# Kernel optimization log

Hardware: AMD Instinct MI355X
Metric: run time of the kernel (lower is better)

The kernel has to match this reference:

```python
import jax, jax.numpy as jnp
import numpy as np

N = 20000       # nodes
E = 320000      # edges
D_IN = 128
H = 512
OUT = 7
EPS = 1e-5


def setup_inputs() -> dict:
    key = jax.random.key(0)
    ks = jax.random.split(key, 16)
    def lin(k, fan_in, fan_out):
        bound = 1.0 / np.sqrt(fan_in)
        kw, kb = jax.random.split(k)
        W = jax.random.uniform(kw, (fan_in, fan_out), jnp.float32, -bound, bound)
        b = jax.random.uniform(kb, (fan_out,), jnp.float32, -bound, bound)
        return W, b
    x = jax.random.normal(ks[0], (N, D_IN), jnp.float32)
    edge_index = jax.random.randint(ks[1], (2, E), 0, N, dtype=jnp.int64)
    W1, b1 = lin(ks[2], D_IN, H)
    W2, b2 = lin(ks[3], H, H)
    W3, b3 = lin(ks[4], H, H)
    W4, b4 = lin(ks[5], H, H)
    ln_gamma = jnp.ones((H,), jnp.float32)
    ln_beta = jnp.zeros((H,), jnp.float32)
    W_out, b_out = lin(ks[6], H, OUT)
    return {"x": x, "edge_index": edge_index,
            "W1": W1, "b1": b1, "W2": W2, "b2": b2,
            "W3": W3, "b3": b3, "W4": W4, "b4": b4,
            "ln_gamma": ln_gamma, "ln_beta": ln_beta,
            "W_out": W_out, "b_out": b_out}


def _gcn_layer(x, W, b, src, dst, dinv):
    # transform, then symmetric-normalized gather/scatter-add (PyG GCNConv)
    h = x @ W                                    # [N, H]
    norm = dinv[src] * dinv[dst]                 # [E+N]
    msg = h[src] * norm[:, None]                 # gather + scale
    agg = jax.ops.segment_sum(msg, dst, num_segments=N)
    return agg + b


def reference(x, edge_index, W1, b1, W2, b2, W3, b3, W4, b4,
              ln_gamma, ln_beta, W_out, b_out):
    loops = jnp.arange(N, dtype=edge_index.dtype)
    src = jnp.concatenate([edge_index[0], loops])  # A + I self loops
    dst = jnp.concatenate([edge_index[1], loops])
    deg = jax.ops.segment_sum(jnp.ones_like(src, dtype=x.dtype), dst,
                              num_segments=N)
    dinv = jnp.where(deg > 0, jax.lax.rsqrt(deg), 0.0)

    def ln(h):
        mu = h.mean(-1, keepdims=True)
        var = h.var(-1, keepdims=True)
        return (h - mu) * jax.lax.rsqrt(var + EPS) * ln_gamma + ln_beta

    for W, b in ((W1, b1), (W2, b2), (W3, b3), (W4, b4)):
        x = jax.nn.relu(ln(_gcn_layer(x, W, b, src, dst, dinv)))
    g = x.mean(axis=0)           # mean pool over nodes -> [H]
    # dropout is identity in eval mode
    return g @ W_out + b_out     # [OUT]
```

## Files before the change

### kernel.cpp

```cpp
#include <hip/hip_runtime.h>

#define HID 512
#define OUTD 7
#define EPSV 1e-5f
#define PB 256
#define PR 32

typedef __attribute__((ext_vector_type(8))) short bf16x8;
typedef __attribute__((ext_vector_type(4))) float f32x4;
typedef __attribute__((ext_vector_type(2))) float f32x2;
typedef unsigned short ushort_t;
typedef unsigned int uint_t;
typedef unsigned char uchar_t;

__device__ __forceinline__ ushort_t f2bf(float f) {
    uint_t u = __float_as_uint(f);
    u = (u + 0x7fffu + ((u >> 16) & 1u)) >> 16;
    return (ushort_t)u;
}
__device__ __forceinline__ float bflo(uint_t u) { return __uint_as_float(u << 16); }
__device__ __forceinline__ float bfhi(uint_t u) { return __uint_as_float(u & 0xffff0000u); }

__device__ __forceinline__ void dec4(uint_t v, float* f) {
    f32x2 p0 = __builtin_amdgcn_cvt_pk_f32_fp8(v, false);
    f32x2 p1 = __builtin_amdgcn_cvt_pk_f32_fp8(v, true);
    f[0] = p0.x; f[1] = p0.y; f[2] = p1.x; f[3] = p1.y;
}
__device__ __forceinline__ uint_t enc4(float a, float b, float c, float d) {
    uint_t r = __builtin_amdgcn_cvt_pk_fp8_f32(a, b, 0, false);
    r = __builtin_amdgcn_cvt_pk_fp8_f32(c, d, r, true);
    return r;
}

__device__ __forceinline__ void gload_lds16(const ushort_t* g, ushort_t* l) {
    __builtin_amdgcn_global_load_lds(
        (const __attribute__((address_space(1))) uint_t*)g,
        (__attribute__((address_space(3))) uint_t*)l, 16, 0, 0);
}
__device__ __forceinline__ void gload_lds16_u8(const uchar_t* g, uchar_t* l) {
    __builtin_amdgcn_global_load_lds(
        (const __attribute__((address_space(1))) uint_t*)g,
        (__attribute__((address_space(3))) uint_t*)l, 16, 0, 0);
}


__global__ void zero_deg(int* __restrict__ deg, int N) {
    int i = blockIdx.x * blockDim.x + threadIdx.x;
    if (i < N) deg[i] = 0;
}

__global__ void setup2(const int* __restrict__ dst, int* __restrict__ deg, int E,
                       const float* __restrict__ W0, const float* __restrict__ W1,
                       const float* __restrict__ W2, const float* __restrict__ W3,
                       ushort_t* __restrict__ T0, ushort_t* __restrict__ T1,
                       ushort_t* __restrict__ T2, ushort_t* __restrict__ T3) {
    int i = blockIdx.x * blockDim.x + threadIdx.x;
    if (i < E) { atomicAdd(&deg[dst[i]], 1); return; }
    i -= E;
    const int S0 = 128 * HID, S1 = HID * HID;
    if (i < S0) { int k = i / HID, n = i % HID; T0[(size_t)n * 128 + k] = f2bf(W0[i]); return; }
    i -= S0;
    if (i < S1) { int k = i / HID, n = i % HID; T1[(size_t)n * HID + k] = f2bf(W1[i]); return; }
    i -= S1;
    if (i < S1) { int k = i / HID, n = i % HID; T2[(size_t)n * HID + k] = f2bf(W2[i]); return; }
    i -= S1;
    if (i < S1) { int k = i / HID, n = i % HID; T3[(size_t)n * HID + k] = f2bf(W3[i]); }
}


__global__ void scan1(const int* __restrict__ deg, int* __restrict__ off,
                      int* __restrict__ partial, float* __restrict__ dinv, int N) {
    __shared__ int s[256];
    const int t = threadIdx.x;
    const int i = blockIdx.x * 256 + t;
    int d = (i < N) ? deg[i] : 0;
    if (i < N) dinv[i] = rsqrtf((float)(d + 1));
    s[t] = d;
    __syncthreads();
#pragma unroll
    for (int ofs = 1; ofs < 256; ofs <<= 1) {
        int v = (t >= ofs) ? s[t - ofs] : 0;
        __syncthreads();
        s[t] += v;
        __syncthreads();
    }
    if (i < N) off[i] = s[t] - d;
    if (t == 255) partial[blockIdx.x] = s[255];
}

__global__ void scan23(int* __restrict__ off, const int* __restrict__ partial,
                       int* __restrict__ cursor, int N, int E, int nb) {
    __shared__ int s[256];
    __shared__ int ex[256];
    const int t = threadIdx.x;
    int d = (t < nb) ? partial[t] : 0;
    s[t] = d;
    __syncthreads();
#pragma unroll
    for (int ofs = 1; ofs < 256; ofs <<= 1) {
        int v = (t >= ofs) ? s[t - ofs] : 0;
        __syncthreads();
        s[t] += v;
        __syncthreads();
    }
    ex[t] = s[t] - d;
    __syncthreads();
    int i = blockIdx.x * 256 + t;
    if (i < N) {
        int v = off[i] + ex[i >> 8];
        off[i] = v;
        cursor[i] = v;
    } else if (i == N) {
        off[N] = E;
    }
}


__global__ void fill_cvt(const int* __restrict__ src, const int* __restrict__ dst,
                         int* __restrict__ cursor, int* __restrict__ srcs, int E,
                         const float* __restrict__ x, const float* __restrict__ dinv,
                         ushort_t* __restrict__ xb, int pairs) {
    int i = blockIdx.x * blockDim.x + threadIdx.x;
    if (i < E) { int p = atomicAdd(&cursor[dst[i]], 1); srcs[p] = src[i]; return; }
    i -= E;
    if (i < pairs) {
        float dr = dinv[i >> 6];
        float a = x[2 * i] * dr, b = x[2 * i + 1] * dr;
        uint_t d = __builtin_amdgcn_cvt_pk_fp8_f32(a, b, 0, false);
        xb[i] = (ushort_t)(d & 0xffffu);
    }
}


__global__ __launch_bounds__(256) void csr_agg_512(
        const uchar_t* __restrict__ xs, const int* __restrict__ off,
        const int* __restrict__ srcs, const float* __restrict__ dinv,
        uchar_t* __restrict__ ax, int N) {
    int gtid = blockIdx.x * 256 + threadIdx.x;
    int r = gtid >> 6, lane = gtid & 63;
    if (r >= N) return;
    const int half = lane >> 5, l32 = lane & 31;
    const uint4* xb = (const uint4*)xs;
    float a[16];
    if (half == 0) {
        uint4 v = xb[(size_t)r * 32 + l32];
        dec4(v.x, a); dec4(v.y, a + 4); dec4(v.z, a + 8); dec4(v.w, a + 12);
    } else {
#pragma unroll
        for (int q = 0; q < 16; q++) a[q] = 0.f;
    }
    int e = off[r];
    const int e1 = off[r + 1];
    for (; e + 8 <= e1; e += 8) {
        int si[4]; uint4 vi[4];
#pragma unroll
        for (int j = 0; j < 4; j++) si[j] = srcs[e + 2 * j + half];
#pragma unroll
        for (int j = 0; j < 4; j++) vi[j] = xb[(size_t)si[j] * 32 + l32];
#pragma unroll
        for (int j = 0; j < 4; j++) {
            float f[16];
            dec4(vi[j].x, f); dec4(vi[j].y, f + 4); dec4(vi[j].z, f + 8); dec4(vi[j].w, f + 12);
#pragma unroll
            for (int q = 0; q < 16; q++) a[q] += f[q];
        }
    }
    for (; e < e1; e += 2) {
        int idx = e + half;
        bool valid = idx < e1;
        int s = srcs[valid ? idx : e];
        uint4 v = xb[(size_t)s * 32 + l32];
        if (!valid) { v.x = 0; v.y = 0; v.z = 0; v.w = 0; }
        float f[16];
        dec4(v.x, f); dec4(v.y, f + 4); dec4(v.z, f + 8); dec4(v.w, f + 12);
#pragma unroll
        for (int q = 0; q < 16; q++) a[q] += f[q];
    }
#pragma unroll
    for (int q = 0; q < 16; q++) a[q] += __shfl_xor(a[q], 32);
    if (half == 0) {
        float dr = dinv[r];
        uint4 o;
        o.x = enc4(a[0] * dr,  a[1] * dr,  a[2] * dr,  a[3] * dr);
        o.y = enc4(a[4] * dr,  a[5] * dr,  a[6] * dr,  a[7] * dr);
        o.z = enc4(a[8] * dr,  a[9] * dr,  a[10] * dr, a[11] * dr);
        o.w = enc4(a[12] * dr, a[13] * dr, a[14] * dr, a[15] * dr);
        ((uint4*)ax)[(size_t)r * 32 + l32] = o;
    }
}

__global__ __launch_bounds__(256) void csr_agg_128(
        const uchar_t* __restrict__ xs, const int* __restrict__ off,
        const int* __restrict__ srcs, const float* __restrict__ dinv,
        uchar_t* __restrict__ ax, int N) {
    int gtid = blockIdx.x * 256 + threadIdx.x;
    int r = gtid >> 6, lane = gtid & 63;
    if (r >= N) return;
    const int sub = lane >> 3, l8 = lane & 7;
    const uint4* xb = (const uint4*)xs;
    float a[16];
    if (sub == 0) {
        uint4 v = xb[(size_t)r * 8 + l8];
        dec4(v.x, a); dec4(v.y, a + 4); dec4(v.z, a + 8); dec4(v.w, a + 12);
    } else {
#pragma unroll
        for (int q = 0; q < 16; q++) a[q] = 0.f;
    }
    const int e1 = off[r + 1];
    for (int e = off[r]; e < e1; e += 8) {
        int idx = e + sub;
        bool valid = idx < e1;
        int s = srcs[valid ? idx : e];
        uint4 v = xb[(size_t)s * 8 + l8];
        if (!valid) { v.x = 0; v.y = 0; v.z = 0; v.w = 0; }
        float f[16];
        dec4(v.x, f); dec4(v.y, f + 4); dec4(v.z, f + 8); dec4(v.w, f + 12);
#pragma unroll
        for (int q = 0; q < 16; q++) a[q] += f[q];
    }
#pragma unroll
    for (int q = 0; q < 16; q++) a[q] += __shfl_xor(a[q], 8);
#pragma unroll
    for (int q = 0; q < 16; q++) a[q] += __shfl_xor(a[q], 16);
#pragma unroll
    for (int q = 0; q < 16; q++) a[q] += __shfl_xor(a[q], 32);
    if (sub == 0) {
        float dr = dinv[r];
        uint4 o;
        o.x = enc4(a[0] * dr,  a[1] * dr,  a[2] * dr,  a[3] * dr);
        o.y = enc4(a[4] * dr,  a[5] * dr,  a[6] * dr,  a[7] * dr);
        o.z = enc4(a[8] * dr,  a[9] * dr,  a[10] * dr, a[11] * dr);
        o.w = enc4(a[12] * dr, a[13] * dr, a[14] * dr, a[15] * dr);
        ((uint4*)ax)[(size_t)r * 8 + l8] = o;
    }
}


__global__ __launch_bounds__(256) void gemm_mfma(
        const uchar_t* __restrict__ A, const ushort_t* __restrict__ Wt,
        const float* __restrict__ bias, ushort_t* __restrict__ C, int M, int K, int MB) {
    __shared__ __align__(16) uchar_t  As[4 * 128 * 16];
    __shared__ __align__(16) ushort_t Bs[8 * 128 * 8];
    const int id = blockIdx.x;
    const int mb = (id >> 5) * 8 + (id & 7);
    const int nbk = (id >> 3) & 3;
    if (mb >= MB) return;
    const int t = threadIdx.x;
    const int wave = t >> 6, lane = t & 63;
    const int m0 = mb * 128, n0 = nbk * 128;
    const int wm = (wave & 1) * 64, wn = (wave >> 1) * 64;
    const int quad = lane >> 4, l16 = lane & 15;

    f32x4 acc[4][4];
#pragma unroll
    for (int i = 0; i < 4; i++)
#pragma unroll
        for (int j = 0; j < 4; j++) acc[i][j] = (f32x4){0.f, 0.f, 0.f, 0.f};

    for (int k0 = 0; k0 < K; k0 += 64) {
#pragma unroll
        for (int h = 0; h < 2; h++) {
            int gm = m0 + 64 * h + lane;
            if (gm >= M) gm = M - 1;
            gload_lds16_u8(A + (size_t)gm * K + k0 + wave * 16,
                           &As[(wave * 128 + 64 * h) * 16]);
        }
#pragma unroll
        for (int h = 0; h < 4; h++) {
            int cb = wave * 2 + (h >> 1);
            int row = (h & 1) * 64 + lane;
            gload_lds16(Wt + (size_t)(n0 + row) * K + k0 + cb * 8,
                        &Bs[(cb * 128 + (h & 1) * 64) * 8]);
        }
        __syncthreads();
#pragma unroll
        for (int kk = 0; kk < 2; kk++) {
            bf16x8 af[4], bfr[4];
#pragma unroll
            for (int jn = 0; jn < 4; jn++)
                bfr[jn] = *(const bf16x8*)&Bs[((kk * 4 + quad) * 128 + wn + jn * 16 + l16) * 8];
#pragma unroll
            for (int i = 0; i < 4; i++) {
                uint2 v8 = *(const uint2*)&As[((kk * 2 + (quad >> 1)) * 128 + wm + i * 16 + l16) * 16
                                              + (quad & 1) * 8];
                f32x2 p0 = __builtin_amdgcn_cvt_pk_f32_fp8(v8.x, false);
                f32x2 p1 = __builtin_amdgcn_cvt_pk_f32_fp8(v8.x, true);
                f32x2 p2 = __builtin_amdgcn_cvt_pk_f32_fp8(v8.y, false);
                f32x2 p3 = __builtin_amdgcn_cvt_pk_f32_fp8(v8.y, true);
                union { uint_t u[4]; bf16x8 v; } pk;
                pk.u[0] = (__float_as_uint(p0.y) & 0xffff0000u) | (__float_as_uint(p0.x) >> 16);
                pk.u[1] = (__float_as_uint(p1.y) & 0xffff0000u) | (__float_as_uint(p1.x) >> 16);
                pk.u[2] = (__float_as_uint(p2.y) & 0xffff0000u) | (__float_as_uint(p2.x) >> 16);
                pk.u[3] = (__float_as_uint(p3.y) & 0xffff0000u) | (__float_as_uint(p3.x) >> 16);
                af[i] = pk.v;
            }
#pragma unroll
            for (int i = 0; i < 4; i++)
#pragma unroll
                for (int jn = 0; jn < 4; jn++)
                    acc[i][jn] = __builtin_amdgcn_mfma_f32_16x16x32_bf16(
                                     af[i], bfr[jn], acc[i][jn], 0, 0, 0);
        }
        __syncthreads();
    }
#pragma unroll
    for (int i = 0; i < 4; i++) {
#pragma unroll
        for (int jn = 0; jn < 4; jn++) {
            int gn = n0 + wn + jn * 16 + l16;
            float bv = bias[gn];
#pragma unroll
            for (int rg = 0; rg < 4; rg++) {
                int gm = m0 + wm + i * 16 + quad * 4 + rg;
                if (gm < M) C[(size_t)gm * HID + gn] = f2bf(acc[i][jn][rg] + bv);
            }
        }
    }
}


__global__ void ln_relu(const ushort_t* __restrict__ h, const float* __restrict__ gamma,
                        const float* __restrict__ beta, const float* __restrict__ dinv,
                        void* __restrict__ optr, int N) {
    int gtid = blockIdx.x * blockDim.x + threadIdx.x;
    int r = gtid >> 6, lane = gtid & 63;
    if (r >= N) return;
    uint4 v = ((const uint4*)(h + (size_t)r * HID))[lane];
    float f[8] = {bflo(v.x), bfhi(v.x), bflo(v.y), bfhi(v.y),
                  bflo(v.z), bfhi(v.z), bflo(v.w), bfhi(v.w)};
    float s = 0.f, q = 0.f;
#pragma unroll
    for (int j = 0; j < 8; j++) { s += f[j]; q += f[j] * f[j]; }
#pragma unroll
    for (int ofs = 32; ofs > 0; ofs >>= 1) {
        s += __shfl_xor(s, ofs);
        q += __shfl_xor(q, ofs);
    }
    float mu  = s * (1.0f / HID);
    float var = q * (1.0f / HID) - mu * mu;
    float rs  = rsqrtf(var + EPSV);
    float dr  = dinv[r];
    const float4* gp = (const float4*)gamma;
    const float4* bp = (const float4*)beta;
    float4 g0 = gp[2 * lane], g1 = gp[2 * lane + 1];
    float4 b0 = bp[2 * lane], b1 = bp[2 * lane + 1];
    float gg[8] = {g0.x, g0.y, g0.z, g0.w, g1.x, g1.y, g1.z, g1.w};
    float bb[8] = {b0.x, b0.y, b0.z, b0.w, b1.x, b1.y, b1.z, b1.w};
    float o[8];
#pragma unroll
    for (int j = 0; j < 8; j++)
        o[j] = fmaxf((f[j] - mu) * rs * gg[j] + bb[j], 0.f) * dr;
    uint2 ov;
    ov.x = enc4(o[0], o[1], o[2], o[3]);
    ov.y = enc4(o[4], o[5], o[6], o[7]);
    ((uint2*)optr)[(size_t)r * 64 + lane] = ov;
}


__global__ __launch_bounds__(256) void ln_pool(
        const ushort_t* __restrict__ h, const float* __restrict__ gamma,
        const float* __restrict__ beta, float* __restrict__ pbuf, int N) {
    __shared__ float sred[4][64][8];
    const int t = threadIdx.x;
    const int sub = t >> 6, lane = t & 63;
    const float4* gp = (const float4*)gamma;
    const float4* bp = (const float4*)beta;
    float4 g0 = gp[2 * lane], g1 = gp[2 * lane + 1];
    float4 b0 = bp[2 * lane], b1 = bp[2 * lane + 1];
    float gg[8] = {g0.x, g0.y, g0.z, g0.w, g1.x, g1.y, g1.z, g1.w};
    float bb[8] = {b0.x, b0.y, b0.z, b0.w, b1.x, b1.y, b1.z, b1.w};
    float colacc[8] = {0.f, 0.f, 0.f, 0.f, 0.f, 0.f, 0.f, 0.f};
    const int step = PB * 4;
    for (int r = blockIdx.x * 4 + sub; r < N; r += step) {
        uint4 v = ((const uint4*)(h + (size_t)r * HID))[lane];
        float f[8] = {bflo(v.x), bfhi(v.x), bflo(v.y), bfhi(v.y),
                      bflo(v.z), bfhi(v.z), bflo(v.w), bfhi(v.w)};
        float s = 0.f, q = 0.f;
#pragma unroll
        for (int j = 0; j < 8; j++) { s += f[j]; q += f[j] * f[j]; }
#pragma unroll
        for (int ofs = 32; ofs > 0; ofs >>= 1) {
            s += __shfl_xor(s, ofs);
            q += __shfl_xor(q, ofs);
        }
        float mu  = s * (1.0f / HID);
        float var = q * (1.0f / HID) - mu * mu;
        float rs  = rsqrtf(var + EPSV);
#pragma unroll
        for (int j = 0; j < 8; j++)
            colacc[j] += fmaxf((f[j] - mu) * rs * gg[j] + bb[j], 0.f);
    }
#pragma unroll
    for (int j = 0; j < 8; j++) sred[sub][lane][j] = colacc[j];
    __syncthreads();
    if (sub == 0) {
        float4 o0, o1;
        o0.x = sred[0][lane][0] + sred[1][lane][0] + sred[2][lane][0] + sred[3][lane][0];
        o0.y = sred[0][lane][1] + sred[1][lane][1] + sred[2][lane][1] + sred[3][lane][1];
        o0.z = sred[0][lane][2] + sred[1][lane][2] + sred[2][lane][2] + sred[3][lane][2];
        o0.w = sred[0][lane][3] + sred[1][lane][3] + sred[2][lane][3] + sred[3][lane][3];
        o1.x = sred[0][lane][4] + sred[1][lane][4] + sred[2][lane][4] + sred[3][lane][4];
        o1.y = sred[0][lane][5] + sred[1][lane][5] + sred[2][lane][5] + sred[3][lane][5];
        o1.z = sred[0][lane][6] + sred[1][lane][6] + sred[2][lane][6] + sred[3][lane][6];
        o1.w = sred[0][lane][7] + sred[1][lane][7] + sred[2][lane][7] + sred[3][lane][7];
        float* pb = pbuf + (size_t)blockIdx.x * HID + lane * 8;
        ((float4*)pb)[0] = o0;
        ((float4*)pb)[1] = o1;
    }
}


__global__ __launch_bounds__(256) void pool_reduce(
        const float* __restrict__ pbuf, float* __restrict__ pbuf2) {
    const int t = threadIdx.x;
    const int b = blockIdx.x;
    const int R = PB / PR;
    float2 s = make_float2(0.f, 0.f);
#pragma unroll
    for (int u = 0; u < R; u++) {
        const float2 v = ((const float2*)(pbuf + (size_t)(b * R + u) * HID))[t];
        s.x += v.x; s.y += v.y;
    }
    ((float2*)(pbuf2 + (size_t)b * HID))[t] = s;
}


__global__ void out_kernel(const float* __restrict__ pbuf2, const float* __restrict__ Wout,
                           const float* __restrict__ bout, float* __restrict__ out, int N) {
    __shared__ float red[256];
    int t = threadIdx.x;
    float g0 = 0.f, g1 = 0.f;
#pragma unroll
    for (int p = 0; p < PR; p += 8) {
#pragma unroll
        for (int u = 0; u < 8; u++) {
            const float2 v = ((const float2*)(pbuf2 + (size_t)(p + u) * HID))[t];
            g0 += v.x; g1 += v.y;
        }
    }
    float invn = 1.0f / (float)N;
    for (int o = 0; o < OUTD; o++) {
        float pr = g0 * Wout[(2 * t) * OUTD + o] + g1 * Wout[(2 * t + 1) * OUTD + o];
        red[t] = pr;
        __syncthreads();
        for (int sft = 128; sft > 0; sft >>= 1) {
            if (t < sft) red[t] += red[t + sft];
            __syncthreads();
        }
        if (t == 0) out[o] = red[0] * invn + bout[o];
        __syncthreads();
    }
}


extern "C" void kernel_launch(void* const* d_in, const int* in_sizes, int n_in,
                              void* d_out, int out_size, void* d_ws, size_t ws_size,
                              hipStream_t stream) {
    const float* x  = (const float*)d_in[0];
    const int*   ei = (const int*)d_in[1];
    const int N = in_sizes[0] / 128;
    const int E = in_sizes[1] / 2;
    const int* src = ei;
    const int* dst = ei + E;
    const float* Ws[4] = {(const float*)d_in[2], (const float*)d_in[4],
                          (const float*)d_in[6], (const float*)d_in[8]};
    const float* bs[4] = {(const float*)d_in[3], (const float*)d_in[5],
                          (const float*)d_in[7], (const float*)d_in[9]};
    const float* gamma = (const float*)d_in[10];
    const float* beta  = (const float*)d_in[11];
    const float* Wout  = (const float*)d_in[12];
    const float* bout  = (const float*)d_in[13];
    float* out = (float*)d_out;

    char* p = (char*)d_ws;
    uchar_t*  axb = (uchar_t*)p;   p += (size_t)N * HID;
    ushort_t* hb  = (ushort_t*)p;  p += sizeof(ushort_t) * (size_t)N * HID;
    uchar_t*  ho8 = (uchar_t*)p;   p += (size_t)N * HID;
    uchar_t*  xb8 = ho8;
    ushort_t* Wt[4];
    Wt[0] = (ushort_t*)p;          p += sizeof(ushort_t) * 128 * HID;
    Wt[1] = (ushort_t*)p;          p += sizeof(ushort_t) * HID * HID;
    Wt[2] = (ushort_t*)p;          p += sizeof(ushort_t) * HID * HID;
    Wt[3] = (ushort_t*)p;          p += sizeof(ushort_t) * HID * HID;
    float* dinv  = (float*)p;      p += sizeof(float) * N;
    float* pbuf  = (float*)p;      p += sizeof(float) * PB * HID;
    float* pbuf2 = (float*)p;      p += sizeof(float) * PR * HID;
    int* deg    = (int*)p;         p += sizeof(int) * N;
    int* off    = (int*)p;         p += sizeof(int) * (N + 4);
    int* cursor = (int*)p;         p += sizeof(int) * N;
    int* partial= (int*)p;         p += sizeof(int) * 256;
    int* srcs   = (int*)p;

    const int nb = (N + 255) / 256;
    const int MB = (N + 127) / 128;
    const int gemm_blocks = 32 * ((MB + 7) / 8);

    zero_deg<<<(N + 255) / 256, 256, 0, stream>>>(deg, N);
    {
        int tot = E + 128 * HID + 3 * HID * HID;
        setup2<<<(tot + 255) / 256, 256, 0, stream>>>(dst, deg, E, Ws[0], Ws[1], Ws[2], Ws[3],
                                                      Wt[0], Wt[1], Wt[2], Wt[3]);
    }
    scan1<<<nb, 256, 0, stream>>>(deg, off, partial, dinv, N);
    scan23<<<(N + 256) / 256, 256, 0, stream>>>(off, partial, cursor, N, E, nb);
    {
        int pairs = N * 64;
        int tot = E + pairs;
        fill_cvt<<<(tot + 255) / 256, 256, 0, stream>>>(src, dst, cursor, srcs, E,
                                                        x, dinv, (ushort_t*)xb8, pairs);
    }

    for (int l = 0; l < 4; l++) {
        const int K = (l == 0) ? 128 : HID;
        if (l == 0)
            csr_agg_128<<<(N * 64 + 255) / 256, 256, 0, stream>>>(xb8, off, srcs, dinv, axb, N);
        else
            csr_agg_512<<<(N * 64 + 255) / 256, 256, 0, stream>>>(ho8, off, srcs, dinv, axb, N);
        gemm_mfma<<<gemm_blocks, 256, 0, stream>>>(axb, Wt[l], bs[l], hb, N, K, MB);
        if (l < 3)
            ln_relu<<<(N * 64 + 255) / 256, 256, 0, stream>>>(hb, gamma, beta, dinv, ho8, N);
        else
            ln_pool<<<PB, 256, 0, stream>>>(hb, gamma, beta, pbuf, N);
    }
    pool_reduce<<<PR, 256, 0, stream>>>(pbuf, pbuf2);
    out_kernel<<<1, 256, 0, stream>>>(pbuf2, Wout, bout, out, N);
}
```

Measured before the change: 372.1 us.

## Tile weight transpose through LDS, split degree count, deepen edge-gather unrolling

The setup kernel that mixed degree atomics with an element-wise, uncoalesced weight transpose is split into a degree-count kernel and a 32x32 LDS-tiled transpose. The tiled transpose uses coalesced float4 reads and ushort4 writes. Zeroing of the degree array now uses hipMemsetAsync instead of a kernel. Both CSR aggregation kernels also get a deeper unrolled main loop (16 edges per iteration) to keep more gathers in flight, at the cost of higher register pressure and an extra kernel launch.

```diff
diff --git a/kernel.cpp b/kernel.cpp
--- a/kernel.cpp
+++ b/kernel.cpp
@@ -44,27 +44,35 @@
 }
 
 
-__global__ void zero_deg(int* __restrict__ deg, int N) {
-    int i = blockIdx.x * blockDim.x + threadIdx.x;
-    if (i < N) deg[i] = 0;
-}
-
-__global__ void setup2(const int* __restrict__ dst, int* __restrict__ deg, int E,
-                       const float* __restrict__ W0, const float* __restrict__ W1,
-                       const float* __restrict__ W2, const float* __restrict__ W3,
-                       ushort_t* __restrict__ T0, ushort_t* __restrict__ T1,
-                       ushort_t* __restrict__ T2, ushort_t* __restrict__ T3) {
-    int i = blockIdx.x * blockDim.x + threadIdx.x;
-    if (i < E) { atomicAdd(&deg[dst[i]], 1); return; }
-    i -= E;
-    const int S0 = 128 * HID, S1 = HID * HID;
-    if (i < S0) { int k = i / HID, n = i % HID; T0[(size_t)n * 128 + k] = f2bf(W0[i]); return; }
-    i -= S0;
-    if (i < S1) { int k = i / HID, n = i % HID; T1[(size_t)n * HID + k] = f2bf(W1[i]); return; }
-    i -= S1;
-    if (i < S1) { int k = i / HID, n = i % HID; T2[(size_t)n * HID + k] = f2bf(W2[i]); return; }
-    i -= S1;
-    if (i < S1) { int k = i / HID, n = i % HID; T3[(size_t)n * HID + k] = f2bf(W3[i]); }
+__global__ void deg_count(const int* __restrict__ dst, int* __restrict__ deg, int E) {
+    int e = blockIdx.x * blockDim.x + threadIdx.x;
+    if (e < E) atomicAdd(&deg[dst[e]], 1);
+}
+
+__global__ __launch_bounds__(256) void wtrans(
+        const float* __restrict__ W0, const float* __restrict__ W1,
+        const float* __restrict__ W2, const float* __restrict__ W3,
+        ushort_t* __restrict__ T0, ushort_t* __restrict__ T1,
+        ushort_t* __restrict__ T2, ushort_t* __restrict__ T3) {
+    __shared__ ushort_t tile[32][33];
+    int id = blockIdx.x;
+    const float* W; ushort_t* T; int K;
+    if (id < 64)       { W = W0; T = T0; K = 128; }
+    else if (id < 320) { W = W1; T = T1; K = 512; id -= 64; }
+    else if (id < 576) { W = W2; T = T2; K = 512; id -= 320; }
+    else               { W = W3; T = T3; K = 512; id -= 576; }
+    const int tn = id & 15;
+    const int tk = id >> 4;
+    const int t = threadIdx.x;
+    const int r = t >> 3;
+    const int c4 = (t & 7) * 4;
+    const float4 v = *(const float4*)&W[(size_t)(tk * 32 + r) * HID + tn * 32 + c4];
+    tile[r][c4 + 0] = f2bf(v.x); tile[r][c4 + 1] = f2bf(v.y);
+    tile[r][c4 + 2] = f2bf(v.z); tile[r][c4 + 3] = f2bf(v.w);
+    __syncthreads();
+    ushort4 ov = make_ushort4(tile[c4 + 0][r], tile[c4 + 1][r],
+                              tile[c4 + 2][r], tile[c4 + 3][r]);
+    *(ushort4*)&T[(size_t)(tn * 32 + r) * K + tk * 32 + c4] = ov;
 }
 
 
@@ -151,6 +159,20 @@
     }
     int e = off[r];
     const int e1 = off[r + 1];
+    for (; e + 16 <= e1; e += 16) {
+        int si[8]; uint4 vi[8];
+#pragma unroll
+        for (int j = 0; j < 8; j++) si[j] = srcs[e + 2 * j + half];
+#pragma unroll
+        for (int j = 0; j < 8; j++) vi[j] = xb[(size_t)si[j] * 32 + l32];
+#pragma unroll
+        for (int j = 0; j < 8; j++) {
+            float f[16];
+            dec4(vi[j].x, f); dec4(vi[j].y, f + 4); dec4(vi[j].z, f + 8); dec4(vi[j].w, f + 12);
+#pragma unroll
+            for (int q = 0; q < 16; q++) a[q] += f[q];
+        }
+    }
     for (; e + 8 <= e1; e += 8) {
         int si[4]; uint4 vi[4];
 #pragma unroll
@@ -206,8 +228,21 @@
 #pragma unroll
         for (int q = 0; q < 16; q++) a[q] = 0.f;
     }
+    int e = off[r];
     const int e1 = off[r + 1];
-    for (int e = off[r]; e < e1; e += 8) {
+    for (; e + 16 <= e1; e += 16) {
+        int s0 = srcs[e + sub], s1 = srcs[e + 8 + sub];
+        uint4 v0 = xb[(size_t)s0 * 8 + l8];
+        uint4 v1 = xb[(size_t)s1 * 8 + l8];
+        float f[16];
+        dec4(v0.x, f); dec4(v0.y, f + 4); dec4(v0.z, f + 8); dec4(v0.w, f + 12);
+#pragma unroll
+        for (int q = 0; q < 16; q++) a[q] += f[q];
+        dec4(v1.x, f); dec4(v1.y, f + 4); dec4(v1.z, f + 8); dec4(v1.w, f + 12);
+#pragma unroll
+        for (int q = 0; q < 16; q++) a[q] += f[q];
+    }
+    for (; e < e1; e += 8) {
         int idx = e + sub;
         bool valid = idx < e1;
         int s = srcs[valid ? idx : e];
@@ -495,12 +530,10 @@
     const int MB = (N + 127) / 128;
     const int gemm_blocks = 32 * ((MB + 7) / 8);
 
-    zero_deg<<<(N + 255) / 256, 256, 0, stream>>>(deg, N);
-    {
-        int tot = E + 128 * HID + 3 * HID * HID;
-        setup2<<<(tot + 255) / 256, 256, 0, stream>>>(dst, deg, E, Ws[0], Ws[1], Ws[2], Ws[3],
-                                                      Wt[0], Wt[1], Wt[2], Wt[3]);
-    }
+    hipMemsetAsync(deg, 0, sizeof(int) * N, stream);
+    deg_count<<<(E + 255) / 256, 256, 0, stream>>>(dst, deg, E);
+    wtrans<<<832, 256, 0, stream>>>(Ws[0], Ws[1], Ws[2], Ws[3],
+                                    Wt[0], Wt[1], Wt[2], Wt[3]);
     scan1<<<nb, 256, 0, stream>>>(deg, off, partial, dinv, N);
     scan23<<<(N + 256) / 256, 256, 0, stream>>>(off, partial, cursor, N, E, nb);
     {
```

Measured after the change: 394.1 us. 1.06x slower.
